# Performance work log

Hardware: AMD Instinct MI355X
Metric: run time of the kernel (lower is better)

The kernel has to match this reference:

```python
import jax, jax.numpy as jnp
import numpy as np

N, IN, H1, H2, E, NE = 32768, 768, 2048, 1024, 64, 256
K_PAIRS, T_TRIP = 4096, 8192
TEMP, MARGIN, BETA = 0.1, 0.2, 0.001


def setup_inputs() -> dict:
    key = jax.random.key(0)
    ks = jax.random.split(key, 18)

    def w(k, i, o):
        return (jax.random.normal(k, (i, o), jnp.float32) / np.sqrt(i)).astype(jnp.float32)

    return {
        'x': jax.random.normal(ks[0], (N, IN), jnp.float32),
        'q_embs': jax.random.normal(ks[1], (N, IN), jnp.float32),
        'qd_align_w': jax.random.uniform(ks[2], (N,), jnp.float32),
        'pairs': jax.random.randint(ks[3], (K_PAIRS, 2), 0, N, jnp.int32),
        'triplets': jax.random.randint(ks[4], (T_TRIP, 3), 0, N, jnp.int32),
        'enc_w0': w(ks[5], IN, H1), 'enc_b0': jnp.zeros((H1,), jnp.float32),
        'enc_w1': w(ks[6], H1, H2), 'enc_b1': jnp.zeros((H2,), jnp.float32),
        'enc_w2': w(ks[7], H2, E), 'enc_b2': jnp.zeros((E,), jnp.float32),
        'dec_w0': w(ks[8], E, H2), 'dec_b0': jnp.zeros((H2,), jnp.float32),
        'dec_w1': w(ks[9], H2, H1), 'dec_b1': jnp.zeros((H1,), jnp.float32),
        'dec_w2': w(ks[10], H1, IN), 'dec_b2': jnp.zeros((IN,), jnp.float32),
        'codebook': w(ks[11], NE, E),
    }


def _mlp(h, w0, b0, w1, b1, w2, b2):
    h = jax.nn.relu(h @ w0 + b0)
    h = jax.nn.relu(h @ w1 + b1)
    return h @ w2 + b2


def _vqvae_forward(x, q_embs, qd_align_w, pairs, triplets,
                   enc_w0, enc_b0, enc_w1, enc_b1, enc_w2, enc_b2,
                   dec_w0, dec_b0, dec_w1, dec_b1, dec_w2, dec_b2, codebook):
    sg = jax.lax.stop_gradient
    # encoder on items and queries
    z = _mlp(x, enc_w0, enc_b0, enc_w1, enc_b1, enc_w2, enc_b2)            # [N, E]
    qz = _mlp(q_embs, enc_w0, enc_b0, enc_w1, enc_b1, enc_w2, enc_b2)      # [N, E]
    # vector quantize: nearest codebook entry
    d = (jnp.sum(z * z, axis=1, keepdims=True)
         - 2.0 * (z @ codebook.T)
         + jnp.sum(codebook * codebook, axis=1))                           # [N, NE]
    idx = jnp.argmin(d, axis=1)                                            # [N]
    x_q = codebook[idx]                                                    # [N, E]
    vq_loss = jnp.mean((x_q - sg(z)) ** 2) + BETA * jnp.mean((sg(x_q) - z) ** 2)
    x_q_st = z + sg(x_q - z)                                               # straight-through
    out = _mlp(x_q_st, dec_w0, dec_b0, dec_w1, dec_b1, dec_w2, dec_b2)     # [N, IN]
    # qd align: weighted cosine similarity between item and query encodings
    cos = jnp.sum(z * qz, axis=-1) / jnp.maximum(
        jnp.linalg.norm(z, axis=-1) * jnp.linalg.norm(qz, axis=-1), 1e-8)
    qd_align_loss = 1.0 - jnp.mean(qd_align_w * cos)
    # outer contrastive (InfoNCE over all rows; pos col replaces itself so
    # CE over [pos, all-but-pos] == logsumexp(all) - pos)
    xn = x_q_st / jnp.maximum(jnp.linalg.norm(x_q_st, axis=1, keepdims=True), 1e-12)
    sim = (xn[pairs[:, 0]] @ xn.T) / TEMP                                  # [K, N]
    pos = jnp.take_along_axis(sim, pairs[:, 1:2].astype(jnp.int32), axis=1)[:, 0]
    outer_con_loss = jnp.mean(jax.nn.logsumexp(sim, axis=1) - pos)
    # inner triplet loss on encoder features
    a, p, n = z[triplets[:, 0]], z[triplets[:, 1]], z[triplets[:, 2]]
    dp = jnp.sqrt(jnp.sum((a - p) ** 2, axis=-1) + 1e-12)
    dn = jnp.sqrt(jnp.sum((a - n) ** 2, axis=-1) + 1e-12)
    inner_triplet_loss = jnp.mean(jax.nn.relu(dp - dn + MARGIN))
    return out, vq_loss, idx[:, None], x_q_st, outer_con_loss, inner_triplet_loss, qd_align_loss


def reference(x, q_embs, qd_align_w, pairs, triplets,
              enc_w0, enc_b0, enc_w1, enc_b1, enc_w2, enc_b2,
              dec_w0, dec_b0, dec_w1, dec_b1, dec_w2, dec_b2, codebook):
    return _vqvae_forward(x, q_embs, qd_align_w, pairs, triplets,
                          enc_w0, enc_b0, enc_w1, enc_b1, enc_w2, enc_b2,
                          dec_w0, dec_b0, dec_w1, dec_b1, dec_w2, dec_b2, codebook)
```

## Files before the change

kernel.cpp:

```cpp
#include <hip/hip_runtime.h>
#include <hip/hip_bf16.h>

namespace {
constexpr int kN = 32768, kIN = 768, kH1 = 2048, kH2 = 1024, kE = 64, kNE = 256;
constexpr int kKP = 4096, kTT = 8192;
constexpr int kCh = 4096;
constexpr int kMaxFix = 4096;

constexpr size_t OFF_OUT = 0;
constexpr size_t OFF_VQ  = (size_t)kN * kIN;
constexpr size_t OFF_IDX = OFF_VQ + 1;
constexpr size_t OFF_XQ  = OFF_IDX + (size_t)kN;
constexpr size_t OFF_OCL = OFF_XQ + (size_t)kN * kE;
constexpr size_t OFF_ITL = OFF_OCL + 1;
constexpr size_t OFF_QDA = OFF_ITL + 1;
}

typedef short bf16x8 __attribute__((ext_vector_type(8)));
typedef float f32x4 __attribute__((ext_vector_type(4)));

__device__ __forceinline__ unsigned short f2bf(float v) {
  __hip_bfloat16 h = __float2bfloat16(v);
  return *reinterpret_cast<unsigned short*>(&h);
}
__device__ __forceinline__ float bf2f(unsigned short u) {
  __hip_bfloat16 h = *reinterpret_cast<__hip_bfloat16*>(&u);
  return __bfloat162float(h);
}

__device__ __forceinline__ void gload_lds16(const void* g, void* lds) {
  __builtin_amdgcn_global_load_lds(
      (const __attribute__((address_space(1))) void*)g,
      (__attribute__((address_space(3))) void*)lds, 16, 0, 0);
}

template <int BM, int BN, int BK, bool RELU, bool OUTF, bool OUTB>
__global__ __launch_bounds__(256) void gemm_bt(const unsigned short* __restrict__ A,
                                               const unsigned short* __restrict__ Bt,
                                               const float* __restrict__ bias,
                                               float* __restrict__ Cf,
                                               unsigned short* __restrict__ Cb,
                                               int N, int K) {
  constexpr int WM = BM / 2, WN = BN / 2, TMt = WM / 16, TNt = WN / 16;
  constexpr int CH = BK / 8;
  constexpr int RA = BM * BK / 2048, RB = BN * BK / 2048;
  __shared__ unsigned short As[BM * BK];
  __shared__ unsigned short Bs[BN * BK];
  const int tid = threadIdx.x, lane = tid & 63, wave = tid >> 6;
  const int wm = (wave >> 1) * WM, wn = (wave & 1) * WN;
  const int l15 = lane & 15, quad = lane >> 4;
  const int rowA0 = blockIdx.y * BM, colB0 = blockIdx.x * BN;
  f32x4 acc[TMt][TNt];
#pragma unroll
  for (int i = 0; i < TMt; ++i)
#pragma unroll
    for (int j = 0; j < TNt; ++j) acc[i][j] = (f32x4){0.f, 0.f, 0.f, 0.f};

  const char* Ab = (const char*)A;
  const char* Bb = (const char*)Bt;
  char* AsB = (char*)As;
  char* BsB = (char*)Bs;

  for (int k0 = 0; k0 < K; k0 += BK) {
    if (k0) __syncthreads();
#pragma unroll
    for (int r = 0; r < RA; ++r) {
      int off = (r * 256 + tid) * 16;
      int row = off / (BK * 2);
      int sc = ((off >> 4) ^ row) & (CH - 1);
      gload_lds16(Ab + (size_t)(rowA0 + row) * (K * 2) + (size_t)k0 * 2 + sc * 16,
                  AsB + off);
    }
#pragma unroll
    for (int r = 0; r < RB; ++r) {
      int off = (r * 256 + tid) * 16;
      int row = off / (BK * 2);
      int sc = ((off >> 4) ^ row) & (CH - 1);
      gload_lds16(Bb + (size_t)(colB0 + row) * (K * 2) + (size_t)k0 * 2 + sc * 16,
                  BsB + off);
    }
    __syncthreads();
#pragma unroll
    for (int ks = 0; ks < BK; ks += 32) {
      bf16x8 af[TMt], bfr[TNt];
#pragma unroll
      for (int i = 0; i < TMt; ++i) {
        int row = wm + i * 16 + l15;
        int c = (((ks >> 3) + quad) ^ row) & (CH - 1);
        af[i] = *(const bf16x8*)(AsB + row * (BK * 2) + c * 16);
      }
#pragma unroll
      for (int j = 0; j < TNt; ++j) {
        int col = wn + j * 16 + l15;
        int c = (((ks >> 3) + quad) ^ col) & (CH - 1);
        bfr[j] = *(const bf16x8*)(BsB + col * (BK * 2) + c * 16);
      }
#pragma unroll
      for (int i = 0; i < TMt; ++i)
#pragma unroll
        for (int j = 0; j < TNt; ++j)
          acc[i][j] = __builtin_amdgcn_mfma_f32_16x16x32_bf16(af[i], bfr[j],
                                                              acc[i][j], 0, 0, 0);
    }
  }
#pragma unroll
  for (int j = 0; j < TNt; ++j) {
    int col = colB0 + wn + j * 16 + l15;
    float bv = bias[col];
#pragma unroll
    for (int i = 0; i < TMt; ++i) {
      int rbase = rowA0 + wm + i * 16 + quad * 4;
#pragma unroll
      for (int r = 0; r < 4; ++r) {
        float v = acc[i][j][r] + bv;
        if (RELU) v = fmaxf(v, 0.f);
        size_t o = (size_t)(rbase + r) * N + col;
        if (OUTF) Cf[o] = v;
        if (OUTB) Cb[o] = f2bf(v);
      }
    }
  }
}

template <int BM, int BN, int BK, bool RELU, int OM>
__global__ __launch_bounds__(256) void gemm_bt_split(
    const unsigned short* __restrict__ Ah, const unsigned short* __restrict__ Al,
    const unsigned short* __restrict__ Bh, const unsigned short* __restrict__ Bl,
    const float* __restrict__ bias, float* __restrict__ Cf,
    unsigned short* __restrict__ Ch, unsigned short* __restrict__ Cl,
    int N, int K) {
  constexpr int WM = BM / 2, WN = BN / 2, TMt = WM / 16, TNt = WN / 16;
  constexpr int CH = BK / 8;
  constexpr int RA = BM * BK / 2048, RB = BN * BK / 2048;
  __shared__ unsigned short AsH[BM * BK];
  __shared__ unsigned short AsL[BM * BK];
  __shared__ unsigned short BsH[BN * BK];
  __shared__ unsigned short BsL[BN * BK];
  const int tid = threadIdx.x, lane = tid & 63, wave = tid >> 6;
  const int wm = (wave >> 1) * WM, wn = (wave & 1) * WN;
  const int l15 = lane & 15, quad = lane >> 4;
  const int rowA0 = blockIdx.y * BM, colB0 = blockIdx.x * BN;
  f32x4 acc[TMt][TNt];
#pragma unroll
  for (int i = 0; i < TMt; ++i)
#pragma unroll
    for (int j = 0; j < TNt; ++j) acc[i][j] = (f32x4){0.f, 0.f, 0.f, 0.f};

  const char* AhB = (const char*)Ah;
  const char* AlB = (const char*)Al;
  const char* BhB = (const char*)Bh;
  const char* BlB = (const char*)Bl;

  for (int k0 = 0; k0 < K; k0 += BK) {
    if (k0) __syncthreads();
#pragma unroll
    for (int r = 0; r < RA; ++r) {
      int off = (r * 256 + tid) * 16;
      int row = off / (BK * 2);
      int sc = ((off >> 4) ^ row) & (CH - 1);
      size_t go = (size_t)(rowA0 + row) * (K * 2) + (size_t)k0 * 2 + sc * 16;
      gload_lds16(AhB + go, (char*)AsH + off);
      gload_lds16(AlB + go, (char*)AsL + off);
    }
#pragma unroll
    for (int r = 0; r < RB; ++r) {
      int off = (r * 256 + tid) * 16;
      int row = off / (BK * 2);
      int sc = ((off >> 4) ^ row) & (CH - 1);
      size_t go = (size_t)(colB0 + row) * (K * 2) + (size_t)k0 * 2 + sc * 16;
      gload_lds16(BhB + go, (char*)BsH + off);
      gload_lds16(BlB + go, (char*)BsL + off);
    }
    __syncthreads();
#pragma unroll
    for (int ks = 0; ks < BK; ks += 32) {
      bf16x8 ah[TMt], al[TMt], bh[TNt], bl[TNt];
#pragma unroll
      for (int i = 0; i < TMt; ++i) {
        int row = wm + i * 16 + l15;
        int c = (((ks >> 3) + quad) ^ row) & (CH - 1);
        int off = row * (BK * 2) + c * 16;
        ah[i] = *(const bf16x8*)((const char*)AsH + off);
        al[i] = *(const bf16x8*)((const char*)AsL + off);
      }
#pragma unroll
      for (int j = 0; j < TNt; ++j) {
        int col = wn + j * 16 + l15;
        int c = (((ks >> 3) + quad) ^ col) & (CH - 1);
        int off = col * (BK * 2) + c * 16;
        bh[j] = *(const bf16x8*)((const char*)BsH + off);
        bl[j] = *(const bf16x8*)((const char*)BsL + off);
      }
#pragma unroll
      for (int i = 0; i < TMt; ++i)
#pragma unroll
        for (int j = 0; j < TNt; ++j) {
          acc[i][j] = __builtin_amdgcn_mfma_f32_16x16x32_bf16(ah[i], bh[j], acc[i][j], 0, 0, 0);
          acc[i][j] = __builtin_amdgcn_mfma_f32_16x16x32_bf16(ah[i], bl[j], acc[i][j], 0, 0, 0);
          acc[i][j] = __builtin_amdgcn_mfma_f32_16x16x32_bf16(al[i], bh[j], acc[i][j], 0, 0, 0);
        }
    }
  }
#pragma unroll
  for (int j = 0; j < TNt; ++j) {
    int col = colB0 + wn + j * 16 + l15;
    float bv = bias[col];
#pragma unroll
    for (int i = 0; i < TMt; ++i) {
      int rbase = rowA0 + wm + i * 16 + quad * 4;
#pragma unroll
      for (int r = 0; r < 4; ++r) {
        float v = acc[i][j][r] + bv;
        if (RELU) v = fmaxf(v, 0.f);
        size_t o = (size_t)(rbase + r) * N + col;
        if (OM == 0) {
          Cf[o] = v;
        } else {
          unsigned short hi = f2bf(v);
          Ch[o] = hi;
          Cl[o] = f2bf(v - bf2f(hi));
        }
      }
    }
  }
}

__global__ __launch_bounds__(256) void transpose_bf16(const float* __restrict__ W,
                                                      unsigned short* __restrict__ Wt,
                                                      int K, int N) {
  __shared__ float t[32][33];
  int bx = blockIdx.x * 32, by = blockIdx.y * 32;
  int tx = threadIdx.x & 31, ty = threadIdx.x >> 5;
#pragma unroll
  for (int i = 0; i < 32; i += 8)
    t[ty + i][tx] = W[(size_t)(by + ty + i) * N + bx + tx];
  __syncthreads();
#pragma unroll
  for (int i = 0; i < 32; i += 8)
    Wt[(size_t)(bx + ty + i) * K + by + tx] = f2bf(t[tx][ty + i]);
}

__global__ __launch_bounds__(256) void transpose_bf16_split(
    const float* __restrict__ W, unsigned short* __restrict__ Wh,
    unsigned short* __restrict__ Wl, int K, int N) {
  __shared__ float t[32][33];
  int bx = blockIdx.x * 32, by = blockIdx.y * 32;
  int tx = threadIdx.x & 31, ty = threadIdx.x >> 5;
#pragma unroll
  for (int i = 0; i < 32; i += 8)
    t[ty + i][tx] = W[(size_t)(by + ty + i) * N + bx + tx];
  __syncthreads();
#pragma unroll
  for (int i = 0; i < 32; i += 8) {
    float v = t[tx][ty + i];
    unsigned short hi = f2bf(v);
    size_t o = (size_t)(bx + ty + i) * K + by + tx;
    Wh[o] = hi;
    Wl[o] = f2bf(v - bf2f(hi));
  }
}

__global__ __launch_bounds__(256) void conv_bf16(const float* __restrict__ in,
                                                 unsigned short* __restrict__ out,
                                                 int n4) {
  int i = (blockIdx.x * 256 + threadIdx.x);
  if (i < n4) {
    float4 v = *(const float4*)(in + (size_t)i * 4);
    unsigned short o[4] = {f2bf(v.x), f2bf(v.y), f2bf(v.z), f2bf(v.w)};
    *(uint2*)(out + (size_t)i * 4) = *(uint2*)o;
  }
}

__global__ __launch_bounds__(256) void conv_split(const float* __restrict__ in,
                                                  unsigned short* __restrict__ oh,
                                                  unsigned short* __restrict__ ol,
                                                  int n4) {
  int i = (blockIdx.x * 256 + threadIdx.x);
  if (i < n4) {
    float4 v = *(const float4*)(in + (size_t)i * 4);
    unsigned short h[4], l[4];
    float vv[4] = {v.x, v.y, v.z, v.w};
#pragma unroll
    for (int k = 0; k < 4; ++k) {
      h[k] = f2bf(vv[k]);
      l[k] = f2bf(vv[k] - bf2f(h[k]));
    }
    *(uint2*)(oh + (size_t)i * 4) = *(uint2*)h;
    *(uint2*)(ol + (size_t)i * 4) = *(uint2*)l;
  }
}

#define FMA4(a, s, v)              \
  a[0] = fmaf(s, v[0], a[0]);      \
  a[1] = fmaf(s, v[1], a[1]);      \
  a[2] = fmaf(s, v[2], a[2]);      \
  a[3] = fmaf(s, v[3], a[3])

__global__ __launch_bounds__(256) void vq_kernel(const float* __restrict__ z,
                                                 const float* __restrict__ cb,
                                                 float* __restrict__ idx_out,
                                                 float* __restrict__ xq_out,
                                                 unsigned short* __restrict__ xqb_out,
                                                 float* __restrict__ xn_out,
                                                 float* __restrict__ acc,
                                                 int* __restrict__ flags,
                                                 int* __restrict__ flagcnt) {
  __shared__ float cbT[kE * kNE];
  const int t = threadIdx.x;
  {
    const f32x4* src = (const f32x4*)(cb + (size_t)t * kE);
#pragma unroll
    for (int q = 0; q < 16; ++q) {
      f32x4 v = src[q];
      cbT[(4 * q + 0) * kNE + t] = v[0];
      cbT[(4 * q + 1) * kNE + t] = v[1];
      cbT[(4 * q + 2) * kNE + t] = v[2];
      cbT[(4 * q + 3) * kNE + t] = v[3];
    }
  }
  __syncthreads();
  const int l = t & 63, wv = t >> 6;
  f32x4 cn = (f32x4){0.f, 0.f, 0.f, 0.f};
  for (int e = 0; e < kE; ++e) {
    f32x4 cv = *(const f32x4*)&cbT[e * kNE + 4 * l];
    cn[0] = fmaf(cv[0], cv[0], cn[0]);
    cn[1] = fmaf(cv[1], cv[1], cn[1]);
    cn[2] = fmaf(cv[2], cv[2], cn[2]);
    cn[3] = fmaf(cv[3], cv[3], cn[3]);
  }
  const int rowBase = (blockIdx.x * 4 + wv) * 16;
  for (int p = 0; p < 4; ++p) {
    const int ra = rowBase + p * 4;
    f32x4 dt[4];
#pragma unroll
    for (int r = 0; r < 4; ++r) dt[r] = (f32x4){0.f, 0.f, 0.f, 0.f};
#pragma unroll
    for (int e4 = 0; e4 < 16; ++e4) {
      f32x4 c0 = *(const f32x4*)&cbT[(4 * e4 + 0) * kNE + 4 * l];
      f32x4 c1 = *(const f32x4*)&cbT[(4 * e4 + 1) * kNE + 4 * l];
      f32x4 c2 = *(const f32x4*)&cbT[(4 * e4 + 2) * kNE + 4 * l];
      f32x4 c3 = *(const f32x4*)&cbT[(4 * e4 + 3) * kNE + 4 * l];
#pragma unroll
      for (int r = 0; r < 4; ++r) {
        f32x4 zv = *(const f32x4*)(z + (size_t)(ra + r) * kE + e4 * 4);
        FMA4(dt[r], zv[0], c0);
        FMA4(dt[r], zv[1], c1);
        FMA4(dt[r], zv[2], c2);
        FMA4(dt[r], zv[3], c3);
      }
    }
#pragma unroll
    for (int r = 0; r < 4; ++r) {
      const int row = ra + r;
      float d0 = cn[0] - 2.f * dt[r][0];
      float d1 = cn[1] - 2.f * dt[r][1];
      float d2 = cn[2] - 2.f * dt[r][2];
      float d3 = cn[3] - 2.f * dt[r][3];
      float m1 = d0, m2 = 3.4e38f;
      int i1 = 4 * l;
      if (d1 < m1) { m2 = m1; m1 = d1; i1 = 4 * l + 1; } else m2 = fminf(m2, d1);
      if (d2 < m1) { m2 = m1; m1 = d2; i1 = 4 * l + 2; } else m2 = fminf(m2, d2);
      if (d3 < m1) { m2 = m1; m1 = d3; i1 = 4 * l + 3; } else m2 = fminf(m2, d3);
#pragma unroll
      for (int m = 32; m > 0; m >>= 1) {
        float om1 = __shfl_xor(m1, m);
        int oi1 = __shfl_xor(i1, m);
        float om2 = __shfl_xor(m2, m);
        float nm2 = fminf(fminf(m2, om2), fmaxf(m1, om1));
        if (om1 < m1 || (om1 == m1 && oi1 < i1)) { m1 = om1; i1 = oi1; }
        m2 = nm2;
      }
      float zl = z[(size_t)row * kE + l];
      float zn = zl * zl;
#pragma unroll
      for (int m = 32; m > 0; m >>= 1) zn += __shfl_xor(zn, m);
      float tau = 5e-5f * sqrtf(zn);
      if (m2 - m1 < tau) {
        if (l == 0) {
          int slot = atomicAdd(flagcnt, 1);
          flags[slot] = row;
        }
        continue;
      }
      const int best = i1;
      if (l == 0) idx_out[row] = (float)best;
      float xq = cb[(size_t)best * kE + l];
      xq_out[(size_t)row * kE + l] = xq;
      xqb_out[(size_t)row * kE + l] = f2bf(xq);
      float dd = xq - zl;
      float sq = dd * dd;
      float nq = xq * xq;
#pragma unroll
      for (int m = 32; m > 0; m >>= 1) {
        sq += __shfl_xor(sq, m);
        nq += __shfl_xor(nq, m);
      }
      float inv = 1.f / fmaxf(sqrtf(nq), 1e-12f);
      xn_out[(size_t)row * kE + l] = xq * inv;
      if (l == 0) atomicAdd(&acc[row & 255], sq);
    }
  }
}
#undef FMA4

__global__ __launch_bounds__(256) void fix_h1(
    const float* __restrict__ x, const float* __restrict__ ew0,
    const float* __restrict__ eb0, const int* __restrict__ flags,
    const int* __restrict__ flagcnt, float* __restrict__ h1f) {
  constexpr int R = 8, NJC = 8, JC = kH1 / NJC;
  __shared__ float xs[R][kIN];
  const int t = threadIdx.x;
  int cnt = *flagcnt;
  if (cnt > kMaxFix) cnt = kMaxFix;
  const int nrb = (cnt + R - 1) / R;
  const int nwork = nrb * NJC;
  for (int w = blockIdx.x; w < nwork; w += gridDim.x) {
    const int rb = w / NJC, jc = w % NJC;
    const int nr = min(R, cnt - rb * R);
    for (int rr = 0; rr < nr; ++rr) {
      const int r = flags[rb * R + rr];
      for (int q = t; q < kIN; q += 256) xs[rr][q] = x[(size_t)r * kIN + q];
    }
    __syncthreads();
    const int j = jc * JC + t;
    float s[R];
    const float b = eb0[j];
#pragma unroll
    for (int rr = 0; rr < R; ++rr) s[rr] = b;
#pragma unroll 8
    for (int k = 0; k < kIN; ++k) {
      float wv = ew0[(size_t)k * kH1 + j];
#pragma unroll
      for (int rr = 0; rr < R; ++rr) s[rr] = fmaf(xs[rr][k], wv, s[rr]);
    }
    for (int rr = 0; rr < nr; ++rr)
      h1f[(size_t)(rb * R + rr) * kH1 + j] = fmaxf(s[rr], 0.f);
    __syncthreads();
  }
}

__global__ __launch_bounds__(256) void fix_h2(
    const float* __restrict__ h1f, const float* __restrict__ ew1,
    const float* __restrict__ eb1, const int* __restrict__ flagcnt,
    float* __restrict__ h2f) {
  constexpr int R = 4, NJC = 4, JC = kH2 / NJC;
  __shared__ float hs[R][kH1];
  const int t = threadIdx.x;
  int cnt = *flagcnt;
  if (cnt > kMaxFix) cnt = kMaxFix;
  const int nrb = (cnt + R - 1) / R;
  const int nwork = nrb * NJC;
  for (int w = blockIdx.x; w < nwork; w += gridDim.x) {
    const int rb = w / NJC, jc = w % NJC;
    const int nr = min(R, cnt - rb * R);
    for (int rr = 0; rr < nr; ++rr)
      for (int q = t; q < kH1; q += 256)
        hs[rr][q] = h1f[(size_t)(rb * R + rr) * kH1 + q];
    __syncthreads();
    const int j = jc * JC + t;
    float s[R];
    const float b = eb1[j];
#pragma unroll
    for (int rr = 0; rr < R; ++rr) s[rr] = b;
#pragma unroll 8
    for (int k = 0; k < kH1; ++k) {
      float wv = ew1[(size_t)k * kH2 + j];
#pragma unroll
      for (int rr = 0; rr < R; ++rr) s[rr] = fmaf(hs[rr][k], wv, s[rr]);
    }
    for (int rr = 0; rr < nr; ++rr)
      h2f[(size_t)(rb * R + rr) * kH2 + j] = fmaxf(s[rr], 0.f);
    __syncthreads();
  }
}

__global__ __launch_bounds__(256) void fix_z(
    const float* __restrict__ h2f, const float* __restrict__ ew2,
    const float* __restrict__ eb2, const float* __restrict__ cb,
    const int* __restrict__ flags, const int* __restrict__ flagcnt,
    float* __restrict__ z, float* __restrict__ idx_out,
    float* __restrict__ xq_out, unsigned short* __restrict__ xqb_out,
    float* __restrict__ xn_out, float* __restrict__ acc) {
  __shared__ float hrow[kH2];
  __shared__ float sred[256];
  __shared__ float szs[kE];
  __shared__ float rv[256];
  __shared__ int ri[256];
  const int t = threadIdx.x;
  int cnt = *flagcnt;
  if (cnt > kMaxFix) cnt = kMaxFix;
  for (int fi = blockIdx.x; fi < cnt; fi += gridDim.x) {
    const int r = flags[fi];
    for (int q = t; q < kH2; q += 256) hrow[q] = h2f[(size_t)fi * kH2 + q];
    __syncthreads();
    {
      const int j = t & 63, p = t >> 6;
      float s = 0.f;
      for (int k = p * 256; k < p * 256 + 256; ++k)
        s = fmaf(hrow[k], ew2[(size_t)k * kE + j], s);
      sred[t] = s;
      __syncthreads();
      if (t < kE) {
        float zv = sred[t] + sred[t + 64] + sred[t + 128] + sred[t + 192] + eb2[t];
        szs[t] = zv;
        z[(size_t)r * kE + t] = zv;
      }
      __syncthreads();
    }
    {
      float dot = 0.f, nrm = 0.f;
      const float* c = cb + (size_t)t * kE;
#pragma unroll 8
      for (int e = 0; e < kE; ++e) {
        float ce = c[e];
        dot = fmaf(szs[e], ce, dot);
        nrm = fmaf(ce, ce, nrm);
      }
      rv[t] = nrm - 2.f * dot;
      ri[t] = t;
      __syncthreads();
      for (int s = 128; s > 0; s >>= 1) {
        if (t < s) {
          float v2 = rv[t + s];
          int i2 = ri[t + s];
          if (v2 < rv[t] || (v2 == rv[t] && i2 < ri[t])) { rv[t] = v2; ri[t] = i2; }
        }
        __syncthreads();
      }
      const int best = ri[0];
      if (t == 0) idx_out[r] = (float)best;
      if (t < kE) {
        float xq = cb[(size_t)best * kE + t];
        xq_out[(size_t)r * kE + t] = xq;
        xqb_out[(size_t)r * kE + t] = f2bf(xq);
        float dd = xq - szs[t];
        float sq = dd * dd;
        float nq = xq * xq;
#pragma unroll
        for (int m = 32; m > 0; m >>= 1) {
          sq += __shfl_xor(sq, m);
          nq += __shfl_xor(nq, m);
        }
        float inv = 1.f / fmaxf(sqrtf(nq), 1e-12f);
        xn_out[(size_t)r * kE + t] = xq * inv;
        if (t == 0) atomicAdd(&acc[r & 255], sq);
      }
      __syncthreads();
    }
  }
}

__global__ __launch_bounds__(256) void fix_rows(
    const float* __restrict__ x, const float* __restrict__ ew0,
    const float* __restrict__ eb0, const float* __restrict__ ew1,
    const float* __restrict__ eb1, const float* __restrict__ ew2,
    const float* __restrict__ eb2, const float* __restrict__ cb,
    const int* __restrict__ flags, const int* __restrict__ flagcnt,
    float* __restrict__ z, float* __restrict__ idx_out,
    float* __restrict__ xq_out, unsigned short* __restrict__ xqb_out,
    float* __restrict__ xn_out, float* __restrict__ acc) {
  __shared__ float xs[kIN];
  __shared__ float sh1[kH1];
  __shared__ float sh2[kH2];
  __shared__ float sred[256];
  __shared__ float szs[kE];
  __shared__ float rv[256];
  __shared__ int ri[256];
  const int t = threadIdx.x;
  const int cnt = *flagcnt;
  for (int fi = kMaxFix + blockIdx.x; fi < cnt; fi += gridDim.x) {
    const int r = flags[fi];
    for (int q = t; q < kIN; q += 256) xs[q] = x[(size_t)r * kIN + q];
    __syncthreads();
#pragma unroll
    for (int o = 0; o < kH1 / 256; ++o) {
      int j = t + 256 * o;
      float s = eb0[j];
      for (int k = 0; k < kIN; ++k) s = fmaf(xs[k], ew0[(size_t)k * kH1 + j], s);
      sh1[j] = fmaxf(s, 0.f);
    }
    __syncthreads();
#pragma unroll
    for (int o = 0; o < kH2 / 256; ++o) {
      int j = t + 256 * o;
      float s = eb1[j];
      for (int k = 0; k < kH1; ++k) s = fmaf(sh1[k], ew1[(size_t)k * kH2 + j], s);
      sh2[j] = fmaxf(s, 0.f);
    }
    __syncthreads();
    {
      int j = t & 63, p = t >> 6;
      float s = 0.f;
      for (int k = p * 256; k < p * 256 + 256; ++k)
        s = fmaf(sh2[k], ew2[(size_t)k * kE + j], s);
      sred[t] = s;
      __syncthreads();
      if (t < kE) {
        float zv = sred[t] + sred[t + 64] + sred[t + 128] + sred[t + 192] + eb2[t];
        szs[t] = zv;
        z[(size_t)r * kE + t] = zv;
      }
      __syncthreads();
    }
    {
      float dot = 0.f, nrm = 0.f;
      const float* c = cb + (size_t)t * kE;
#pragma unroll 8
      for (int e = 0; e < kE; ++e) {
        float ce = c[e];
        dot = fmaf(szs[e], ce, dot);
        nrm = fmaf(ce, ce, nrm);
      }
      rv[t] = nrm - 2.f * dot;
      ri[t] = t;
      __syncthreads();
      for (int s = 128; s > 0; s >>= 1) {
        if (t < s) {
          float v2 = rv[t + s];
          int i2 = ri[t + s];
          if (v2 < rv[t] || (v2 == rv[t] && i2 < ri[t])) { rv[t] = v2; ri[t] = i2; }
        }
        __syncthreads();
      }
      const int best = ri[0];
      if (t == 0) idx_out[r] = (float)best;
      if (t < kE) {
        float xq = cb[(size_t)best * kE + t];
        xq_out[(size_t)r * kE + t] = xq;
        xqb_out[(size_t)r * kE + t] = f2bf(xq);
        float dd = xq - szs[t];
        float sq = dd * dd;
        float nq = xq * xq;
#pragma unroll
        for (int m = 32; m > 0; m >>= 1) {
          sq += __shfl_xor(sq, m);
          nq += __shfl_xor(nq, m);
        }
        float inv = 1.f / fmaxf(sqrtf(nq), 1e-12f);
        xn_out[(size_t)r * kE + t] = xq * inv;
        if (t == 0) atomicAdd(&acc[r & 255], sq);
      }
      __syncthreads();
    }
  }
}

__global__ __launch_bounds__(256) void qd_kernel(const float* __restrict__ z,
                                                 const float* __restrict__ qz,
                                                 const float* __restrict__ w,
                                                 float* __restrict__ acc) {
  const int i = blockIdx.x * 4 + (threadIdx.x >> 6);
  const int l = threadIdx.x & 63;
  float a = z[(size_t)i * kE + l];
  float b = qz[(size_t)i * kE + l];
  float dot = a * b, na = a * a, nb = b * b;
#pragma unroll
  for (int m = 32; m > 0; m >>= 1) {
    dot += __shfl_xor(dot, m);
    na += __shfl_xor(na, m);
    nb += __shfl_xor(nb, m);
  }
  if (l == 0) {
    float cosv = dot / fmaxf(sqrtf(na) * sqrtf(nb), 1e-8f);
    atomicAdd(&acc[i & 255], w[i] * cosv);
  }
}

__global__ __launch_bounds__(256) void trip_kernel(const float* __restrict__ z,
                                                   const int* __restrict__ tr,
                                                   float* __restrict__ acc) {
  const int t = blockIdx.x * 4 + (threadIdx.x >> 6);
  const int l = threadIdx.x & 63;
  int ia = tr[3 * t], ip = tr[3 * t + 1], in2 = tr[3 * t + 2];
  float a = z[(size_t)ia * kE + l];
  float p = z[(size_t)ip * kE + l];
  float n = z[(size_t)in2 * kE + l];
  float d1 = (a - p) * (a - p);
  float d2 = (a - n) * (a - n);
#pragma unroll
  for (int m = 32; m > 0; m >>= 1) {
    d1 += __shfl_xor(d1, m);
    d2 += __shfl_xor(d2, m);
  }
  if (l == 0) {
    float dp = sqrtf(d1 + 1e-12f);
    float dn = sqrtf(d2 + 1e-12f);
    atomicAdd(&acc[t & 255], fmaxf(dp - dn + 0.2f, 0.f));
  }
}

__global__ __launch_bounds__(256) void pos_kernel(const float* __restrict__ xn,
                                                  const int* __restrict__ pairs,
                                                  float* __restrict__ acc) {
  const int k = blockIdx.x * 4 + (threadIdx.x >> 6);
  const int l = threadIdx.x & 63;
  int i0 = pairs[2 * k], i1 = pairs[2 * k + 1];
  float v = xn[(size_t)i0 * kE + l] * xn[(size_t)i1 * kE + l];
#pragma unroll
  for (int m = 32; m > 0; m >>= 1) v += __shfl_xor(v, m);
  if (l == 0) atomicAdd(&acc[k & 255], -10.f * v);
}


__global__ __launch_bounds__(256) void hist_kernel(const float* __restrict__ idx_out,
                                                   int* __restrict__ cnt) {
  __shared__ int h[kNE];
  const int t = threadIdx.x;
  h[t] = 0;
  __syncthreads();
  int i = blockIdx.x * 256 + t;
  atomicAdd(&h[(int)idx_out[i]], 1);
  __syncthreads();
  if (h[t]) atomicAdd(&cnt[t], h[t]);
}

__global__ __launch_bounds__(256) void code_lse(const float* __restrict__ cb,
                                                const int* __restrict__ cnt,
                                                float* __restrict__ E) {
  __shared__ float cbn[kNE][kE + 1];
  __shared__ float red[256];
  const int t = threadIdx.x, a = blockIdx.x;
  const float* r = cb + (size_t)t * kE;
  float s = 0.f;
#pragma unroll 8
  for (int e = 0; e < kE; ++e) s = fmaf(r[e], r[e], s);
  float inv = 1.f / fmaxf(sqrtf(s), 1e-12f);
#pragma unroll 8
  for (int e = 0; e < kE; ++e) cbn[t][e] = r[e] * inv;
  __syncthreads();
  float dot = 0.f;
#pragma unroll 8
  for (int e = 0; e < kE; ++e) dot = fmaf(cbn[a][e], cbn[t][e], dot);
  red[t] = (float)cnt[t] * expf(10.f * dot);
  __syncthreads();
  for (int sred = 128; sred > 0; sred >>= 1) {
    if (t < sred) red[t] += red[t + sred];
    __syncthreads();
  }
  if (t == 0) E[a] = red[0];
}

__global__ __launch_bounds__(256) void pair_log(const float* __restrict__ idx_out,
                                                const int* __restrict__ pairs,
                                                const float* __restrict__ E,
                                                float* __restrict__ acc) {
  int p = blockIdx.x * 256 + threadIdx.x;
  int a = (int)idx_out[pairs[2 * p]];
  atomicAdd(&acc[p & 255], logf(E[a]));
}

__global__ __launch_bounds__(256) void finalize_kernel(const float* __restrict__ acc,
                                                       float* __restrict__ out) {
  const int t = threadIdx.x;
  float vq = acc[t], qd = acc[256 + t], tr = acc[512 + t], ou = acc[768 + t];
#pragma unroll
  for (int m = 32; m > 0; m >>= 1) {
    vq += __shfl_xor(vq, m);
    qd += __shfl_xor(qd, m);
    tr += __shfl_xor(tr, m);
    ou += __shfl_xor(ou, m);
  }
  __shared__ float sm[4][4];
  const int w = t >> 6;
  if ((t & 63) == 0) { sm[0][w] = vq; sm[1][w] = qd; sm[2][w] = tr; sm[3][w] = ou; }
  __syncthreads();
  if (t == 0) {
    float svq = sm[0][0] + sm[0][1] + sm[0][2] + sm[0][3];
    float sqd = sm[1][0] + sm[1][1] + sm[1][2] + sm[1][3];
    float str = sm[2][0] + sm[2][1] + sm[2][2] + sm[2][3];
    float sou = sm[3][0] + sm[3][1] + sm[3][2] + sm[3][3];
    out[OFF_VQ]  = 1.001f * svq / (float)((size_t)kN * kE);
    out[OFF_OCL] = sou / (float)kKP;
    out[OFF_ITL] = str / (float)kTT;
    out[OFF_QDA] = 1.f - sqd / (float)kN;
  }
}

extern "C" void kernel_launch(void* const* d_in, const int* in_sizes, int n_in,
                              void* d_out, int out_size, void* d_ws, size_t ws_size,
                              hipStream_t stream) {
  (void)in_sizes; (void)n_in; (void)out_size; (void)ws_size;
  const float* x    = (const float*)d_in[0];
  const float* qe   = (const float*)d_in[1];
  const float* qdw  = (const float*)d_in[2];
  const int*   prs  = (const int*)d_in[3];
  const int*   trs  = (const int*)d_in[4];
  const float* ew0  = (const float*)d_in[5];
  const float* eb0  = (const float*)d_in[6];
  const float* ew1  = (const float*)d_in[7];
  const float* eb1  = (const float*)d_in[8];
  const float* ew2  = (const float*)d_in[9];
  const float* eb2  = (const float*)d_in[10];
  const float* dw0  = (const float*)d_in[11];
  const float* db0  = (const float*)d_in[12];
  const float* dw1  = (const float*)d_in[13];
  const float* db1  = (const float*)d_in[14];
  const float* dw2  = (const float*)d_in[15];
  const float* db2  = (const float*)d_in[16];
  const float* cb   = (const float*)d_in[17];
  float* out = (float*)d_out;

  float* z   = (float*)d_ws;
  float* qz  = z  + (size_t)kN * kE;
  float* xn  = qz + (size_t)kN * kE;
  float* acc = xn + (size_t)kN * kE;
  float* pairsum = acc + 1024;
  int*   flagcnt = (int*)(pairsum + 4096);
  int*   flags   = flagcnt + 64;
  unsigned short* xqb  = (unsigned short*)(flags + kN);
  unsigned short* wt0h = xqb  + (size_t)kN * kE;
  unsigned short* wt0l = wt0h + (size_t)kH1 * kIN;
  unsigned short* wt1h = wt0l + (size_t)kH1 * kIN;
  unsigned short* wt1l = wt1h + (size_t)kH2 * kH1;
  unsigned short* wt2h = wt1l + (size_t)kH2 * kH1;
  unsigned short* wt2l = wt2h + (size_t)kE * kH2;
  unsigned short* wt3  = wt2l + (size_t)kE * kH2;
  unsigned short* wt4  = wt3  + (size_t)kH2 * kE;
  unsigned short* wt5  = wt4  + (size_t)kH1 * kH2;
  unsigned short* xh  = wt5 + (size_t)kIN * kH1;
  unsigned short* xl  = xh + (size_t)kCh * kIN;
  unsigned short* h1h = xl + (size_t)kCh * kIN;
  unsigned short* h1l = h1h + (size_t)kCh * kH1;
  unsigned short* h2h = h1l + (size_t)kCh * kH1;
  unsigned short* h2l = h2h + (size_t)kCh * kH2;
  float* h1f = (float*)xh;
  float* h2f = h1f + (size_t)kMaxFix * kH1;
  int*   cnt = (int*)pairsum;
  float* E   = pairsum + 256;

  hipMemsetAsync(acc, 0, (1024 + 4096 + 64) * sizeof(float), stream);

  transpose_bf16_split<<<dim3(kH1 / 32, kIN / 32), 256, 0, stream>>>(ew0, wt0h, wt0l, kIN, kH1);
  transpose_bf16_split<<<dim3(kH2 / 32, kH1 / 32), 256, 0, stream>>>(ew1, wt1h, wt1l, kH1, kH2);
  transpose_bf16_split<<<dim3(kE / 32, kH2 / 32), 256, 0, stream>>>(ew2, wt2h, wt2l, kH2, kE);
  transpose_bf16<<<dim3(kH2 / 32, kE / 32), 256, 0, stream>>>(dw0, wt3, kE, kH2);
  transpose_bf16<<<dim3(kH1 / 32, kH2 / 32), 256, 0, stream>>>(dw1, wt4, kH2, kH1);
  transpose_bf16<<<dim3(kIN / 32, kH1 / 32), 256, 0, stream>>>(dw2, wt5, kH1, kIN);

  for (int c = 0; c < kN / kCh; ++c) {
    conv_split<<<(kCh * kIN / 4 + 255) / 256, 256, 0, stream>>>(
        x + (size_t)c * kCh * kIN, xh, xl, kCh * kIN / 4);
    gemm_bt_split<128, 128, 64, true, 2>
        <<<dim3(kH1 / 128, kCh / 128), 256, 0, stream>>>(
            xh, xl, wt0h, wt0l, eb0, nullptr, h1h, h1l, kH1, kIN);
    gemm_bt_split<128, 128, 64, true, 2>
        <<<dim3(kH2 / 128, kCh / 128), 256, 0, stream>>>(
            h1h, h1l, wt1h, wt1l, eb1, nullptr, h2h, h2l, kH2, kH1);
    gemm_bt_split<128, 64, 64, false, 0>
        <<<dim3(kE / 64, kCh / 128), 256, 0, stream>>>(
            h2h, h2l, wt2h, wt2l, eb2, z + (size_t)c * kCh * kE, nullptr, nullptr,
            kE, kH2);
  }

  vq_kernel<<<512, 256, 0, stream>>>(z, cb, out + OFF_IDX, out + OFF_XQ, xqb, xn,
                                     acc, flags, flagcnt);
  fix_h1<<<512, 256, 0, stream>>>(x, ew0, eb0, flags, flagcnt, h1f);
  fix_h2<<<512, 256, 0, stream>>>(h1f, ew1, eb1, flagcnt, h2f);
  fix_z<<<512, 256, 0, stream>>>(h2f, ew2, eb2, cb, flags, flagcnt, z,
                                 out + OFF_IDX, out + OFF_XQ, xqb, xn, acc);
  fix_rows<<<64, 256, 0, stream>>>(x, ew0, eb0, ew1, eb1, ew2, eb2, cb, flags,
                                   flagcnt, z, out + OFF_IDX, out + OFF_XQ, xqb,
                                   xn, acc);

  for (int c = 0; c < kN / kCh; ++c) {
    gemm_bt<128, 128, 64, true, false, true>
        <<<dim3(kH2 / 128, kCh / 128), 256, 0, stream>>>(
            xqb + (size_t)c * kCh * kE, wt3, db0, nullptr, h2h, kH2, kE);
    gemm_bt<128, 128, 64, true, false, true>
        <<<dim3(kH1 / 128, kCh / 128), 256, 0, stream>>>(
            h2h, wt4, db1, nullptr, h1h, kH1, kH2);
    gemm_bt<128, 128, 64, false, true, false>
        <<<dim3(kIN / 128, kCh / 128), 256, 0, stream>>>(
            h1h, wt5, db2, out + OFF_OUT + (size_t)c * kCh * kIN, nullptr, kIN, kH1);
  }

  for (int c = 0; c < kN / kCh; ++c) {
    conv_bf16<<<(kCh * kIN / 4 + 255) / 256, 256, 0, stream>>>(
        qe + (size_t)c * kCh * kIN, xh, kCh * kIN / 4);
    gemm_bt<128, 128, 64, true, false, true>
        <<<dim3(kH1 / 128, kCh / 128), 256, 0, stream>>>(
            xh, wt0h, eb0, nullptr, h1h, kH1, kIN);
    gemm_bt<128, 128, 64, true, false, true>
        <<<dim3(kH2 / 128, kCh / 128), 256, 0, stream>>>(
            h1h, wt1h, eb1, nullptr, h2h, kH2, kH1);
    gemm_bt<128, 64, 64, false, true, false>
        <<<dim3(kE / 64, kCh / 128), 256, 0, stream>>>(
            h2h, wt2h, eb2, qz + (size_t)c * kCh * kE, nullptr, kE, kH2);
  }

  qd_kernel<<<kN / 4, 256, 0, stream>>>(z, qz, qdw, acc + 256);
  trip_kernel<<<kTT / 4, 256, 0, stream>>>(z, trs, acc + 512);
  pos_kernel<<<kKP / 4, 256, 0, stream>>>(xn, prs, acc + 768);
  hist_kernel<<<kN / 256, 256, 0, stream>>>(out + OFF_IDX, cnt);
  code_lse<<<kNE, 256, 0, stream>>>(cb, cnt, E);
  pair_log<<<kKP / 256, 256, 0, stream>>>(out + OFF_IDX, prs, E, acc + 768);

  finalize_kernel<<<1, 256, 0, stream>>>(acc, out);
}
```

Baseline: 2.988 ms.

## Add XCD block swizzle, widen VQ row tile, and rewrite fp32 fix MLP kernels

```diff
diff --git a/kernel.cpp b/kernel.cpp
--- a/kernel.cpp
+++ b/kernel.cpp
@@ -32,6 +32,17 @@
   __builtin_amdgcn_global_load_lds(
       (const __attribute__((address_space(1))) void*)g,
       (__attribute__((address_space(3))) void*)lds, 16, 0, 0);
+}
+
+__device__ __forceinline__ void xcd_swizzle(int& bx, int& by) {
+  int gx = gridDim.x, gy = gridDim.y;
+  int nwg = gx * gy;
+  if (nwg & 7) return;
+  int bid = by * gx + bx;
+  int cpx = nwg >> 3;
+  int swz = (bid & 7) * cpx + (bid >> 3);
+  bx = swz % gx;
+  by = swz / gx;
 }
 
 template <int BM, int BN, int BK, bool RELU, bool OUTF, bool OUTB>
@@ -49,7 +60,9 @@
   const int tid = threadIdx.x, lane = tid & 63, wave = tid >> 6;
   const int wm = (wave >> 1) * WM, wn = (wave & 1) * WN;
   const int l15 = lane & 15, quad = lane >> 4;
-  const int rowA0 = blockIdx.y * BM, colB0 = blockIdx.x * BN;
+  int bxs = blockIdx.x, bys = blockIdx.y;
+  xcd_swizzle(bxs, bys);
+  const int rowA0 = bys * BM, colB0 = bxs * BN;
   f32x4 acc[TMt][TNt];
 #pragma unroll
   for (int i = 0; i < TMt; ++i)
@@ -139,7 +152,9 @@
   const int tid = threadIdx.x, lane = tid & 63, wave = tid >> 6;
   const int wm = (wave >> 1) * WM, wn = (wave & 1) * WN;
   const int l15 = lane & 15, quad = lane >> 4;
-  const int rowA0 = blockIdx.y * BM, colB0 = blockIdx.x * BN;
+  int bxs = blockIdx.x, bys = blockIdx.y;
+  xcd_swizzle(bxs, bys);
+  const int rowA0 = bys * BM, colB0 = bxs * BN;
   f32x4 acc[TMt][TNt];
 #pragma unroll
   for (int i = 0; i < TMt; ++i)
@@ -329,11 +344,11 @@
     cn[3] = fmaf(cv[3], cv[3], cn[3]);
   }
   const int rowBase = (blockIdx.x * 4 + wv) * 16;
-  for (int p = 0; p < 4; ++p) {
-    const int ra = rowBase + p * 4;
-    f32x4 dt[4];
-#pragma unroll
-    for (int r = 0; r < 4; ++r) dt[r] = (f32x4){0.f, 0.f, 0.f, 0.f};
+  for (int p = 0; p < 2; ++p) {
+    const int ra = rowBase + p * 8;
+    f32x4 dt[8];
+#pragma unroll
+    for (int r = 0; r < 8; ++r) dt[r] = (f32x4){0.f, 0.f, 0.f, 0.f};
 #pragma unroll
     for (int e4 = 0; e4 < 16; ++e4) {
       f32x4 c0 = *(const f32x4*)&cbT[(4 * e4 + 0) * kNE + 4 * l];
@@ -341,7 +356,7 @@
       f32x4 c2 = *(const f32x4*)&cbT[(4 * e4 + 2) * kNE + 4 * l];
       f32x4 c3 = *(const f32x4*)&cbT[(4 * e4 + 3) * kNE + 4 * l];
 #pragma unroll
-      for (int r = 0; r < 4; ++r) {
+      for (int r = 0; r < 8; ++r) {
         f32x4 zv = *(const f32x4*)(z + (size_t)(ra + r) * kE + e4 * 4);
         FMA4(dt[r], zv[0], c0);
         FMA4(dt[r], zv[1], c1);
@@ -350,7 +365,7 @@
       }
     }
 #pragma unroll
-    for (int r = 0; r < 4; ++r) {
+    for (int r = 0; r < 8; ++r) {
       const int row = ra + r;
       float d0 = cn[0] - 2.f * dt[r][0];
       float d1 = cn[1] - 2.f * dt[r][1];
@@ -403,74 +418,83 @@
 }
 #undef FMA4
 
-__global__ __launch_bounds__(256) void fix_h1(
-    const float* __restrict__ x, const float* __restrict__ ew0,
-    const float* __restrict__ eb0, const int* __restrict__ flags,
-    const int* __restrict__ flagcnt, float* __restrict__ h1f) {
-  constexpr int R = 8, NJC = 8, JC = kH1 / NJC;
-  __shared__ float xs[R][kIN];
+template <int K, int OUTN, bool GATHER>
+__global__ __launch_bounds__(256) void fix_mlp(
+    const float* __restrict__ X, const float* __restrict__ W,
+    const float* __restrict__ bias, const int* __restrict__ flags,
+    const int* __restrict__ flagcnt, float* __restrict__ H) {
+  constexpr int R = 16, JC = 64, KC = 256;
+  constexpr int NJC = OUTN / JC;
+  constexpr int NKC = K / KC;
+  constexpr int PAD = 20;
+  __shared__ float xs[KC * PAD];
+  __shared__ float red[4 * R * JC];
   const int t = threadIdx.x;
+  const int lane = t & 63, w = t >> 6;
   int cnt = *flagcnt;
   if (cnt > kMaxFix) cnt = kMaxFix;
   const int nrb = (cnt + R - 1) / R;
   const int nwork = nrb * NJC;
-  for (int w = blockIdx.x; w < nwork; w += gridDim.x) {
-    const int rb = w / NJC, jc = w % NJC;
-    const int nr = min(R, cnt - rb * R);
-    for (int rr = 0; rr < nr; ++rr) {
-      const int r = flags[rb * R + rr];
-      for (int q = t; q < kIN; q += 256) xs[rr][q] = x[(size_t)r * kIN + q];
+  for (int item = blockIdx.x; item < nwork; item += gridDim.x) {
+    const int rb = item / NJC, jc = item % NJC;
+    const int j = jc * JC + lane;
+    float acc[R];
+#pragma unroll
+    for (int r = 0; r < R; ++r) acc[r] = 0.f;
+    for (int kc = 0; kc < NKC; ++kc) {
+      __syncthreads();
+      for (int i = t; i < R * KC; i += 256) {
+        int r = i >> 8;
+        int k = i & 255;
+        int row = rb * R + r;
+        if (row >= cnt) row = cnt - 1;
+        const float* src = GATHER ? (X + (size_t)flags[row] * K)
+                                  : (X + (size_t)row * K);
+        xs[k * PAD + r] = src[kc * KC + k];
+      }
+      __syncthreads();
+      const float* wp = W + (size_t)(kc * KC + w * 64) * OUTN + j;
+#pragma unroll 4
+      for (int k = 0; k < 64; ++k) {
+        float wv = wp[(size_t)k * OUTN];
+        const float* xp = &xs[(w * 64 + k) * PAD];
+        f32x4 x0 = *(const f32x4*)(xp + 0);
+        f32x4 x1 = *(const f32x4*)(xp + 4);
+        f32x4 x2 = *(const f32x4*)(xp + 8);
+        f32x4 x3 = *(const f32x4*)(xp + 12);
+        acc[0] = fmaf(x0[0], wv, acc[0]);
+        acc[1] = fmaf(x0[1], wv, acc[1]);
+        acc[2] = fmaf(x0[2], wv, acc[2]);
+        acc[3] = fmaf(x0[3], wv, acc[3]);
+        acc[4] = fmaf(x1[0], wv, acc[4]);
+        acc[5] = fmaf(x1[1], wv, acc[5]);
+        acc[6] = fmaf(x1[2], wv, acc[6]);
+        acc[7] = fmaf(x1[3], wv, acc[7]);
+        acc[8] = fmaf(x2[0], wv, acc[8]);
+        acc[9] = fmaf(x2[1], wv, acc[9]);
+        acc[10] = fmaf(x2[2], wv, acc[10]);
+        acc[11] = fmaf(x2[3], wv, acc[11]);
+        acc[12] = fmaf(x3[0], wv, acc[12]);
+        acc[13] = fmaf(x3[1], wv, acc[13]);
+        acc[14] = fmaf(x3[2], wv, acc[14]);
+        acc[15] = fmaf(x3[3], wv, acc[15]);
+      }
     }
     __syncthreads();
-    const int j = jc * JC + t;
-    float s[R];
-    const float b = eb0[j];
-#pragma unroll
-    for (int rr = 0; rr < R; ++rr) s[rr] = b;
-#pragma unroll 8
-    for (int k = 0; k < kIN; ++k) {
-      float wv = ew0[(size_t)k * kH1 + j];
-#pragma unroll
-      for (int rr = 0; rr < R; ++rr) s[rr] = fmaf(xs[rr][k], wv, s[rr]);
-    }
-    for (int rr = 0; rr < nr; ++rr)
-      h1f[(size_t)(rb * R + rr) * kH1 + j] = fmaxf(s[rr], 0.f);
+#pragma unroll
+    for (int r = 0; r < R; ++r) red[(w * R + r) * JC + lane] = acc[r];
     __syncthreads();
-  }
-}
-
-__global__ __launch_bounds__(256) void fix_h2(
-    const float* __restrict__ h1f, const float* __restrict__ ew1,
-    const float* __restrict__ eb1, const int* __restrict__ flagcnt,
-    float* __restrict__ h2f) {
-  constexpr int R = 4, NJC = 4, JC = kH2 / NJC;
-  __shared__ float hs[R][kH1];
-  const int t = threadIdx.x;
-  int cnt = *flagcnt;
-  if (cnt > kMaxFix) cnt = kMaxFix;
-  const int nrb = (cnt + R - 1) / R;
-  const int nwork = nrb * NJC;
-  for (int w = blockIdx.x; w < nwork; w += gridDim.x) {
-    const int rb = w / NJC, jc = w % NJC;
-    const int nr = min(R, cnt - rb * R);
-    for (int rr = 0; rr < nr; ++rr)
-      for (int q = t; q < kH1; q += 256)
-        hs[rr][q] = h1f[(size_t)(rb * R + rr) * kH1 + q];
-    __syncthreads();
-    const int j = jc * JC + t;
-    float s[R];
-    const float b = eb1[j];
-#pragma unroll
-    for (int rr = 0; rr < R; ++rr) s[rr] = b;
-#pragma unroll 8
-    for (int k = 0; k < kH1; ++k) {
-      float wv = ew1[(size_t)k * kH2 + j];
-#pragma unroll
-      for (int rr = 0; rr < R; ++rr) s[rr] = fmaf(hs[rr][k], wv, s[rr]);
-    }
-    for (int rr = 0; rr < nr; ++rr)
-      h2f[(size_t)(rb * R + rr) * kH2 + j] = fmaxf(s[rr], 0.f);
-    __syncthreads();
+#pragma unroll
+    for (int r4 = 0; r4 < 4; ++r4) {
+      int r = w * 4 + r4;
+      int row = rb * R + r;
+      if (row < cnt) {
+        float s = bias[j] + red[(0 * R + r) * JC + lane] +
+                  red[(1 * R + r) * JC + lane] + red[(2 * R + r) * JC + lane] +
+                  red[(3 * R + r) * JC + lane];
+        H[(size_t)row * OUTN + j] = fmaxf(s, 0.f);
+      }
+    }
   }
 }
 
@@ -701,7 +725,6 @@
   if (l == 0) atomicAdd(&acc[k & 255], -10.f * v);
 }
 
-
 __global__ __launch_bounds__(256) void hist_kernel(const float* __restrict__ idx_out,
                                                    int* __restrict__ cnt) {
   __shared__ int h[kNE];
@@ -854,8 +877,8 @@
 
   vq_kernel<<<512, 256, 0, stream>>>(z, cb, out + OFF_IDX, out + OFF_XQ, xqb, xn,
                                      acc, flags, flagcnt);
-  fix_h1<<<512, 256, 0, stream>>>(x, ew0, eb0, flags, flagcnt, h1f);
-  fix_h2<<<512, 256, 0, stream>>>(h1f, ew1, eb1, flagcnt, h2f);
+  fix_mlp<kIN, kH1, true><<<1024, 256, 0, stream>>>(x, ew0, eb0, flags, flagcnt, h1f);
+  fix_mlp<kH1, kH2, false><<<1024, 256, 0, stream>>>(h1f, ew1, eb1, flags, flagcnt, h2f);
   fix_z<<<512, 256, 0, stream>>>(h2f, ew2, eb2, cb, flags, flagcnt, z,
                                  out + OFF_IDX, out + OFF_XQ, xqb, xn, acc);
   fix_rows<<<64, 256, 0, stream>>>(x, ew0, eb0, ew1, eb1, ew2, eb2, cb, flags,
```

After: 2.894 ms. 1.03x faster.
